# Kernel tuning notes

Hardware: AMD Instinct MI355X
Metric: run time of the kernel (lower is better)

## Reference

```python
import jax, jax.numpy as jnp
import numpy as np

D_MODEL = 1024
NUM_HEADS = 16
DEPTH = D_MODEL // NUM_HEADS
B, S = 2, 2048


def setup_inputs() -> dict:
    key = jax.random.key(0)
    ks = jax.random.split(key, 12)
    scale = 1.0 / np.sqrt(D_MODEL)
    inp = {
        'q': jax.random.normal(ks[0], (B, S, D_MODEL), dtype=jnp.float32),
        'k': jax.random.normal(ks[1], (B, S, D_MODEL), dtype=jnp.float32),
        'v': jax.random.normal(ks[2], (B, S, D_MODEL), dtype=jnp.float32),
        'mask': jnp.zeros((1, 1, S, S), dtype=jnp.float32),
        'wq': jax.random.normal(ks[3], (D_MODEL, D_MODEL), dtype=jnp.float32) * scale,
        'bq': jnp.zeros((D_MODEL,), dtype=jnp.float32),
        'wk': jax.random.normal(ks[4], (D_MODEL, D_MODEL), dtype=jnp.float32) * scale,
        'bk': jnp.zeros((D_MODEL,), dtype=jnp.float32),
        'wv': jax.random.normal(ks[5], (D_MODEL, D_MODEL), dtype=jnp.float32) * scale,
        'bv': jnp.zeros((D_MODEL,), dtype=jnp.float32),
        'wo': jax.random.normal(ks[6], (D_MODEL, D_MODEL), dtype=jnp.float32) * scale,
        'bo': jnp.zeros((D_MODEL,), dtype=jnp.float32),
    }
    return inp


def _split_heads(x):
    # [B, S, D] -> [B, H, S, depth]
    b, s, _ = x.shape
    return x.reshape(b, s, NUM_HEADS, DEPTH).transpose(0, 2, 1, 3)


def reference(q, k, v, mask, wq, bq, wk, bk, wv, bv, wo, bo):
    qh = _split_heads(q @ wq + bq)   # [B,H,S,depth]
    kh = _split_heads(k @ wk + bk)
    vh = _split_heads(v @ wv + bv)
    logits = jnp.einsum('bhqd,bhkd->bhqk', qh, kh) / jnp.sqrt(jnp.float32(DEPTH))
    logits = logits + mask * (-1e9)
    attn = jax.nn.softmax(logits, axis=-1)
    out = jnp.einsum('bhqk,bhkd->bhqd', attn, vh)  # [B,H,S,depth]
    out = out.transpose(0, 2, 1, 3).reshape(q.shape[0], -1, D_MODEL)
    return out @ wo + bo
```

## Files before the change

kernel.cpp:

```cpp
#include <hip/hip_runtime.h>

typedef unsigned short u16;
typedef unsigned int   u32;
typedef unsigned long long u64;
typedef short s16;

using f32x4  = __attribute__((ext_vector_type(4))) float;
using bf16x8 = __attribute__((ext_vector_type(8))) __bf16;
using bf16x4 = __attribute__((ext_vector_type(4))) __bf16;
using u16x8  = __attribute__((ext_vector_type(8))) u16;
using u16x4  = __attribute__((ext_vector_type(4))) u16;
using s16x4  = __attribute__((ext_vector_type(4))) s16;

#define LOG2E 1.4426950408889634f

__device__ __forceinline__ u16 f2bf(float f) {
  u32 u = __builtin_bit_cast(u32, f);
  u32 r = u + 0x7fffu + ((u >> 16) & 1u);
  return (u16)(r >> 16);
}

__device__ __forceinline__ float ex2(float x) {
#if __has_builtin(__builtin_amdgcn_exp2f)
  return __builtin_amdgcn_exp2f(x);
#else
  return exp2f(x);
#endif
}

__device__ __forceinline__ u16x4 pack4(float p0, float p1, float p2, float p3) {
  bf16x4 b = {(__bf16)p0, (__bf16)p1, (__bf16)p2, (__bf16)p3};
  return __builtin_bit_cast(u16x4, b);
}

__device__ __forceinline__ void gll16(const u16* g, u16* l) {
  __builtin_amdgcn_global_load_lds(
      (const __attribute__((address_space(1))) void*)g,
      (__attribute__((address_space(3))) void*)l, 16, 0, 0);
}

__device__ __forceinline__ bf16x8 ld_bf8(const u16* p) {
  return __builtin_bit_cast(bf16x8, *(const u16x8*)p);
}

__device__ __forceinline__ f32x4 mfma32(bf16x8 a, bf16x8 b, f32x4 c) {
  return __builtin_amdgcn_mfma_f32_16x16x32_bf16(a, b, c, 0, 0, 0);
}

#if __has_builtin(__builtin_amdgcn_mfma_f32_16x16x16bf16_1k)
__device__ __forceinline__ f32x4 pv_mfma(u16x4 a, u16x4 b, f32x4 c) {
  return __builtin_amdgcn_mfma_f32_16x16x16bf16_1k(
      __builtin_bit_cast(s16x4, a), __builtin_bit_cast(s16x4, b), c, 0, 0, 0);
}
#else
__device__ __forceinline__ f32x4 pv_mfma(u16x4 a, u16x4 b, f32x4 c) {
  u16x8 a8 = {a[0], a[1], a[2], a[3], 0, 0, 0, 0};
  u16x8 b8 = {b[0], b[1], b[2], b[3], 0, 0, 0, 0};
  return mfma32(__builtin_bit_cast(bf16x8, a8),
                __builtin_bit_cast(bf16x8, b8), c);
}
#endif

__global__ __launch_bounds__(256) void pre_kernel(
    const float* __restrict__ q, const float* __restrict__ k,
    const float* __restrict__ v, const float* __restrict__ mask,
    const float* __restrict__ wq, const float* __restrict__ wk,
    const float* __restrict__ wv, const float* __restrict__ wo,
    u16* __restrict__ qb, u16* __restrict__ kb, u16* __restrict__ vb,
    u16* __restrict__ wqT, u16* __restrict__ wkT, u16* __restrict__ wvT,
    u16* __restrict__ woT, int* flag) {
  int y = blockIdx.y, t = threadIdx.x;
  if (y < 3) {
    const float* src = y == 0 ? q : y == 1 ? k : v;
    u16* dst = y == 0 ? qb : y == 1 ? kb : vb;
    u64 i = ((u64)blockIdx.x * 256 + t) * 8;
    f32x4 a = *(const f32x4*)(src + i);
    f32x4 b = *(const f32x4*)(src + i + 4);
    u16x8 o;
    o[0] = f2bf(a[0]); o[1] = f2bf(a[1]); o[2] = f2bf(a[2]); o[3] = f2bf(a[3]);
    o[4] = f2bf(b[0]); o[5] = f2bf(b[1]); o[6] = f2bf(b[2]); o[7] = f2bf(b[3]);
    *(u16x8*)(dst + i) = o;
  } else if (y == 3) {
    __shared__ float tile[32][33];
    int x = t & 31, yy = t >> 5;
#pragma unroll
    for (int rep = 0; rep < 2; ++rep) {
      int job = blockIdx.x * 2 + rep;
      int z = job >> 10, tt = job & 1023;
      const float* W = z == 0 ? wq : z == 1 ? wk : z == 2 ? wv : wo;
      u16* WT = z == 0 ? wqT : z == 1 ? wkT : z == 2 ? wvT : woT;
      int c0 = (tt & 31) * 32, r0 = (tt >> 5) * 32;
#pragma unroll
      for (int j = 0; j < 4; ++j)
        tile[yy + j * 8][x] = W[(u64)(r0 + yy + j * 8) * 1024 + c0 + x];
      __syncthreads();
#pragma unroll
      for (int j = 0; j < 4; ++j)
        WT[(u64)(c0 + yy + j * 8) * 1024 + r0 + x] = f2bf(tile[x][yy + j * 8]);
      __syncthreads();
    }
  } else {
    u64 i = ((u64)blockIdx.x * 256 + t) * 8;
    f32x4 a = *(const f32x4*)(mask + i);
    f32x4 b = *(const f32x4*)(mask + i + 4);
    bool nz = a[0] != 0.f || a[1] != 0.f || a[2] != 0.f || a[3] != 0.f ||
              b[0] != 0.f || b[1] != 0.f || b[2] != 0.f || b[3] != 0.f;
    if (nz) atomicOr(flag, 1);
  }
}

__device__ __forceinline__ void gemm_core(const u16* __restrict__ A,
                                          const u16* __restrict__ Wt, int m0,
                                          int n0, u16* As, u16* Bs,
                                          f32x4 acc[4][4]) {
  int t = threadIdx.x, w = t >> 6, lane = t & 63;
  int quad = lane >> 4, l16 = lane & 15;
  int wr = w >> 1, wc = w & 1;
  for (int kt = 0; kt < 1024; kt += 64) {
#pragma unroll
    for (int j = 0; j < 4; ++j) {
      int g = j * 256 + t;
      int row = g >> 3, slot = g & 7;
      int cc = slot ^ (row & 7);
      gll16(A + (u64)(m0 + row) * 1024 + kt + cc * 8, &As[g * 8]);
      gll16(Wt + (u64)(n0 + row) * 1024 + kt + cc * 8, &Bs[g * 8]);
    }
    __syncthreads();
#pragma unroll
    for (int ks = 0; ks < 2; ++ks) {
      bf16x8 af[4], bfr[4];
#pragma unroll
      for (int mi = 0; mi < 4; ++mi) {
        int r = wr * 64 + mi * 16 + l16;
        af[mi] = ld_bf8(&As[(r * 8 + ((ks * 4 + quad) ^ (r & 7))) * 8]);
      }
#pragma unroll
      for (int ni = 0; ni < 4; ++ni) {
        int r = wc * 64 + ni * 16 + l16;
        bfr[ni] = ld_bf8(&Bs[(r * 8 + ((ks * 4 + quad) ^ (r & 7))) * 8]);
      }
#pragma unroll
      for (int mi = 0; mi < 4; ++mi)
#pragma unroll
        for (int ni = 0; ni < 4; ++ni)
          acc[mi][ni] = mfma32(af[mi], bfr[ni], acc[mi][ni]);
    }
    __syncthreads();
  }
}

__global__ __launch_bounds__(256) void qkv_gemm(
    const u16* __restrict__ qb, const u16* __restrict__ kb,
    const u16* __restrict__ vb, const u16* __restrict__ wqT,
    const u16* __restrict__ wkT, const u16* __restrict__ wvT,
    const float* __restrict__ bq, const float* __restrict__ bk,
    const float* __restrict__ bv, u16* __restrict__ Qh,
    u16* __restrict__ Khs, u16* __restrict__ Vhs) {
  int z = blockIdx.z;
  const u16* A = z == 0 ? qb : z == 1 ? kb : vb;
  const u16* Wt = z == 0 ? wqT : z == 1 ? wkT : wvT;
  const float* bias = z == 0 ? bq : z == 1 ? bk : bv;
  int m0 = blockIdx.x * 128, n0 = blockIdx.y * 128;
  __shared__ u16 SH[16384];
  f32x4 acc[4][4] = {};
  gemm_core(A, Wt, m0, n0, SH, SH + 8192, acc);
  int t = threadIdx.x, w = t >> 6, lane = t & 63;
  int quad = lane >> 4, l16 = lane & 15;
  int wr = w >> 1, wc = w & 1;
  int h = (n0 + wc * 64) >> 6;
  if (z == 2) {
#pragma unroll
    for (int mi = 0; mi < 4; ++mi) {
      int gm0 = m0 + wr * 64 + mi * 16;
      int bh = (gm0 >> 11) * 16 + h;
      int tIdx = (gm0 & 2047) >> 6;
      int kvq = ((gm0 & 63) >> 2) + quad;
      u16* tile = Vhs + ((u64)(bh * 32 + tIdx)) * 4096;
#pragma unroll
      for (int ni = 0; ni < 4; ++ni) {
        int d = ni * 16 + l16;
        float bv_ = bias[n0 + wc * 64 + d];
        u16x4 pv = pack4(acc[mi][ni][0] + bv_, acc[mi][ni][1] + bv_,
                         acc[mi][ni][2] + bv_, acc[mi][ni][3] + bv_);
        *(u16x4*)&tile[(kvq * 64 + d) * 4] = pv;
      }
    }
  } else {
    __syncthreads();
    u16* TB = SH + w * 2304;
    float scale = (z == 0) ? (LOG2E / 8.f) : 1.f;
#pragma unroll
    for (int p = 0; p < 2; ++p) {
#pragma unroll
      for (int mi2 = 0; mi2 < 2; ++mi2)
#pragma unroll
        for (int ni = 0; ni < 4; ++ni) {
          int d = ni * 16 + l16;
          float bv_ = bias[n0 + wc * 64 + d];
#pragma unroll
          for (int r = 0; r < 4; ++r) {
            int kvloc = mi2 * 16 + quad * 4 + r;
            TB[kvloc * 72 + d] =
                f2bf((acc[p * 2 + mi2][ni][r] + bv_) * scale);
          }
        }
      int gm0 = m0 + wr * 64 + p * 32;
      int bh = (gm0 >> 11) * 16 + h;
#pragma unroll
      for (int i = 0; i < 4; ++i) {
        int g = i * 64 + lane;
        int kvloc = g >> 3, slot = g & 7;
        if (z == 0) {
          u16x8 gran = *(u16x8*)&TB[kvloc * 72 + slot * 8];
          int s = (gm0 & 2047) + kvloc;
          *(u16x8*)&Qh[((u64)bh * 2048 + s) * 64 + slot * 8] = gran;
        } else {
          u16x8 gran = *(u16x8*)&TB[kvloc * 72 + (slot ^ (kvloc & 7)) * 8];
          int tIdx = (gm0 & 2047) >> 6;
          int kv = (gm0 & 63) + kvloc;
          *(u16x8*)&Khs[((u64)(bh * 32 + tIdx)) * 4096 + kv * 64 + slot * 8] =
              gran;
        }
      }
    }
  }
}

template <int CUR>
__device__ __forceinline__ void fa_fast_step(
    int T, int t, int quad, int l16, int hf, int x7,
    const u16* __restrict__ Kg0, const u16* __restrict__ Vg0, u16* Kb0,
    u16* Vb0, bf16x8 aq0, bf16x8 aq1, f32x4 (&o)[4], f32x4& l_acc,
    const u16x4 ones) {
  if (T + 1 < 32) {
    gll16(Kg0 + (u64)(T + 1) * 4096 + t * 8, &Kb0[(CUR ^ 1) * 4096 + t * 8]);
    gll16(Vg0 + (u64)(T + 1) * 4096 + t * 8, &Vb0[(CUR ^ 1) * 4096 + t * 8]);
  }
  const u16* Kt = Kb0 + CUR * 4096;
  const u16* Vt = Vb0 + CUR * 4096;
  u16x4 pk[2];
#pragma unroll
  for (int c = 0; c < 2; ++c) {
    int kvr = hf * 32 + c * 16 + l16;
    bf16x8 k0 = ld_bf8(&Kt[kvr * 64 + ((quad ^ x7)) * 8]);
    bf16x8 k1 = ld_bf8(&Kt[kvr * 64 + (((quad + 4) ^ x7)) * 8]);
    f32x4 s_ = {};
    s_ = mfma32(k0, aq0, s_);
    s_ = mfma32(k1, aq1, s_);
    pk[c] = pack4(ex2(s_[0]), ex2(s_[1]), ex2(s_[2]), ex2(s_[3]));
  }
#pragma unroll
  for (int c = 0; c < 2; ++c) {
    int cc = hf * 2 + c;
    l_acc = pv_mfma(pk[c], ones, l_acc);
#pragma unroll
    for (int nt = 0; nt < 4; ++nt) {
      u16x4 vf =
          *(const u16x4*)&Vt[(((cc * 4 + quad) * 64) + nt * 16 + l16) * 4];
      o[nt] = pv_mfma(pk[c], vf, o[nt]);
    }
  }
  __syncthreads();
}

template <int CUR>
__device__ __forceinline__ void fa_mask_step(
    int T, int t, int lane, int quad, int l16, int hf, int x7, int qg,
    const u16* __restrict__ Kg0, const u16* __restrict__ Vg0,
    const float* __restrict__ mask, u16* Kb0, u16* Vb0, bf16x8 aq0,
    bf16x8 aq1, f32x4 (&o)[4], float& m_r, float& l_r) {
  if (T + 1 < 32) {
    gll16(Kg0 + (u64)(T + 1) * 4096 + t * 8, &Kb0[(CUR ^ 1) * 4096 + t * 8]);
    gll16(Vg0 + (u64)(T + 1) * 4096 + t * 8, &Vb0[(CUR ^ 1) * 4096 + t * 8]);
  }
  const u16* Kt = Kb0 + CUR * 4096;
  const u16* Vt = Vb0 + CUR * 4096;
  f32x4 sv[2];
#pragma unroll
  for (int c = 0; c < 2; ++c) {
    int kvr = hf * 32 + c * 16 + l16;
    bf16x8 k0 = ld_bf8(&Kt[kvr * 64 + ((quad ^ x7)) * 8]);
    bf16x8 k1 = ld_bf8(&Kt[kvr * 64 + (((quad + 4) ^ x7)) * 8]);
    f32x4 s_ = {};
    s_ = mfma32(k0, aq0, s_);
    s_ = mfma32(k1, aq1, s_);
    sv[c] = s_;
  }
#pragma unroll
  for (int c = 0; c < 2; ++c)
#pragma unroll
    for (int r = 0; r < 4; ++r)
      sv[c][r] += mask[(u64)qg * 2048 + T * 64 + hf * 32 + c * 16 + quad * 4 +
                       r] *
                  (-1e9f * LOG2E);
  float mx = fmaxf(fmaxf(fmaxf(sv[0][0], sv[0][1]), fmaxf(sv[0][2], sv[0][3])),
                   fmaxf(fmaxf(sv[1][0], sv[1][1]), fmaxf(sv[1][2], sv[1][3])));
  mx = fmaxf(mx, __shfl_xor(mx, 16));
  mx = fmaxf(mx, __shfl_xor(mx, 32));
  float mnew = fmaxf(m_r, mx);
  float alpha = ex2(m_r - mnew);
  m_r = mnew;
  float rs = 0.f;
  u16x4 pk[2];
#pragma unroll
  for (int c = 0; c < 2; ++c) {
    float p0 = ex2(sv[c][0] - m_r), p1 = ex2(sv[c][1] - m_r);
    float p2 = ex2(sv[c][2] - m_r), p3 = ex2(sv[c][3] - m_r);
    rs += (p0 + p1) + (p2 + p3);
    pk[c] = pack4(p0, p1, p2, p3);
  }
  rs += __shfl_xor(rs, 16);
  rs += __shfl_xor(rs, 32);
  l_r = l_r * alpha + rs;
  float a4[4];
#pragma unroll
  for (int r = 0; r < 4; ++r)
    a4[r] = __shfl(alpha, (lane & 48) | (quad * 4 + r));
#pragma unroll
  for (int nt = 0; nt < 4; ++nt)
#pragma unroll
    for (int r = 0; r < 4; ++r) o[nt][r] *= a4[r];
#pragma unroll
  for (int c = 0; c < 2; ++c) {
    int cc = hf * 2 + c;
#pragma unroll
    for (int nt = 0; nt < 4; ++nt) {
      u16x4 vf =
          *(const u16x4*)&Vt[(((cc * 4 + quad) * 64) + nt * 16 + l16) * 4];
      o[nt] = pv_mfma(pk[c], vf, o[nt]);
    }
  }
  __syncthreads();
}

__global__ __launch_bounds__(512, 8) void flash_attn(
    const u16* __restrict__ Qh, const u16* __restrict__ Khs,
    const u16* __restrict__ Vhs, const float* __restrict__ mask,
    const int* __restrict__ flag, u16* __restrict__ Ob) {
  int L = blockIdx.x + (blockIdx.y << 5);
  int bh = (L & 7) * 4 + ((L >> 3) & 3);
  int q0 = (L >> 5) * 64;
  int t = threadIdx.x, w = t >> 6, lane = t & 63;
  int quad = lane >> 4, l16 = lane & 15;
  int s = w >> 1, hf = w & 1;
  __shared__ u16 SMEM[16384];
  u16* Kb0 = SMEM;
  u16* Vb0 = SMEM + 8192;
  const u16* Kg0 = Khs + (u64)bh * 32 * 4096;
  const u16* Vg0 = Vhs + (u64)bh * 32 * 4096;
  const u16* Qbase = Qh + ((u64)bh * 2048 + q0 + s * 16 + l16) * 64 + quad * 8;
  bf16x8 aq0 = ld_bf8(Qbase);
  bf16x8 aq1 = ld_bf8(Qbase + 32);
  f32x4 o[4] = {};
  const bool use_mask = (*flag) != 0;
  int x7 = l16 & 7;
  const u16x4 ones = {0x3F80, 0x3F80, 0x3F80, 0x3F80};
  gll16(Kg0 + t * 8, &Kb0[t * 8]);
  gll16(Vg0 + t * 8, &Vb0[t * 8]);
  __syncthreads();
  int b = bh >> 4, h = bh & 15;
  float* scratch = (float*)SMEM;
  float* my = scratch + (s * 64 + lane) * 20;
  if (!use_mask) {
    f32x4 l_acc = {};
    for (int T = 0; T < 32; T += 2) {
      fa_fast_step<0>(T, t, quad, l16, hf, x7, Kg0, Vg0, Kb0, Vb0, aq0, aq1,
                      o, l_acc, ones);
      fa_fast_step<1>(T + 1, t, quad, l16, hf, x7, Kg0, Vg0, Kb0, Vb0, aq0,
                      aq1, o, l_acc, ones);
    }
    if (hf) {
#pragma unroll
      for (int nt = 0; nt < 4; ++nt)
#pragma unroll
        for (int r = 0; r < 4; ++r) my[nt * 4 + r] = o[nt][r];
#pragma unroll
      for (int r = 0; r < 4; ++r) my[16 + r] = l_acc[r];
    }
    __syncthreads();
    if (!hf) {
      float rl[4];
#pragma unroll
      for (int r = 0; r < 4; ++r) rl[r] = 1.f / (l_acc[r] + my[16 + r]);
#pragma unroll
      for (int nt = 0; nt < 4; ++nt)
#pragma unroll
        for (int r = 0; r < 4; ++r) {
          int srow = q0 + s * 16 + quad * 4 + r;
          Ob[(u64)(b * 2048 + srow) * 1024 + h * 64 + nt * 16 + l16] =
              f2bf((o[nt][r] + my[nt * 4 + r]) * rl[r]);
        }
    }
  } else {
    float m_r = -1e30f, l_r = 0.f;
    int qg = q0 + s * 16 + l16;
    for (int T = 0; T < 32; T += 2) {
      fa_mask_step<0>(T, t, lane, quad, l16, hf, x7, qg, Kg0, Vg0, mask, Kb0,
                      Vb0, aq0, aq1, o, m_r, l_r);
      fa_mask_step<1>(T + 1, t, lane, quad, l16, hf, x7, qg, Kg0, Vg0, mask,
                      Kb0, Vb0, aq0, aq1, o, m_r, l_r);
    }
    if (hf) {
#pragma unroll
      for (int nt = 0; nt < 4; ++nt)
#pragma unroll
        for (int r = 0; r < 4; ++r) my[nt * 4 + r] = o[nt][r];
      my[16] = l_r;
      my[17] = m_r;
    }
    __syncthreads();
    if (!hf) {
      float l1 = my[16], m1 = my[17];
      float m = fmaxf(m_r, m1);
      float c0 = ex2(m_r - m), c1 = ex2(m1 - m);
      float l = l_r * c0 + l1 * c1;
      float c0r[4], c1r[4], rl[4];
#pragma unroll
      for (int r = 0; r < 4; ++r) {
        int src = (lane & 48) | (quad * 4 + r);
        c0r[r] = __shfl(c0, src);
        c1r[r] = __shfl(c1, src);
        rl[r] = 1.f / __shfl(l, src);
      }
#pragma unroll
      for (int nt = 0; nt < 4; ++nt)
#pragma unroll
        for (int r = 0; r < 4; ++r) {
          int srow = q0 + s * 16 + quad * 4 + r;
          float val = (o[nt][r] * c0r[r] + my[nt * 4 + r] * c1r[r]) * rl[r];
          Ob[(u64)(b * 2048 + srow) * 1024 + h * 64 + nt * 16 + l16] =
              f2bf(val);
        }
    }
  }
}

__global__ __launch_bounds__(256) void out_gemm(const u16* __restrict__ Ob,
                                                const u16* __restrict__ woT,
                                                const float* __restrict__ bo,
                                                float* __restrict__ out) {
  int m0 = blockIdx.x * 128, n0 = blockIdx.y * 64;
  __shared__ u16 As[128 * 64], Bs[64 * 64];
  f32x4 acc[2][4] = {};
  int t = threadIdx.x, w = t >> 6, lane = t & 63;
  int quad = lane >> 4, l16 = lane & 15;
  for (int kt = 0; kt < 1024; kt += 64) {
#pragma unroll
    for (int j = 0; j < 4; ++j) {
      int g = j * 256 + t;
      int row = g >> 3, slot = g & 7;
      int cc = slot ^ (row & 7);
      gll16(Ob + (u64)(m0 + row) * 1024 + kt + cc * 8, &As[g * 8]);
    }
#pragma unroll
    for (int j = 0; j < 2; ++j) {
      int g = j * 256 + t;
      int row = g >> 3, slot = g & 7;
      int cc = slot ^ (row & 7);
      gll16(woT + (u64)(n0 + row) * 1024 + kt + cc * 8, &Bs[g * 8]);
    }
    __syncthreads();
#pragma unroll
    for (int ks = 0; ks < 2; ++ks) {
      bf16x8 af[2], bfr[4];
#pragma unroll
      for (int mi = 0; mi < 2; ++mi) {
        int r = w * 32 + mi * 16 + l16;
        af[mi] = ld_bf8(&As[(r * 8 + ((ks * 4 + quad) ^ (r & 7))) * 8]);
      }
#pragma unroll
      for (int ni = 0; ni < 4; ++ni) {
        int r = ni * 16 + l16;
        bfr[ni] = ld_bf8(&Bs[(r * 8 + ((ks * 4 + quad) ^ (r & 7))) * 8]);
      }
#pragma unroll
      for (int mi = 0; mi < 2; ++mi)
#pragma unroll
        for (int ni = 0; ni < 4; ++ni)
          acc[mi][ni] = mfma32(af[mi], bfr[ni], acc[mi][ni]);
    }
    __syncthreads();
  }
#pragma unroll
  for (int mi = 0; mi < 2; ++mi) {
#pragma unroll
    for (int ni = 0; ni < 4; ++ni) {
      int gn = n0 + ni * 16 + l16;
      float bv_ = bo[gn];
#pragma unroll
      for (int r = 0; r < 4; ++r) {
        int gm = m0 + w * 32 + mi * 16 + quad * 4 + r;
        out[(u64)gm * 1024 + gn] = acc[mi][ni][r] + bv_;
      }
    }
  }
}

extern "C" void kernel_launch(void* const* d_in, const int* in_sizes, int n_in,
                              void* d_out, int out_size, void* d_ws,
                              size_t ws_size, hipStream_t stream) {
  const float* q = (const float*)d_in[0];
  const float* k = (const float*)d_in[1];
  const float* v = (const float*)d_in[2];
  const float* mask = (const float*)d_in[3];
  const float* wq = (const float*)d_in[4];
  const float* bq = (const float*)d_in[5];
  const float* wk = (const float*)d_in[6];
  const float* bk = (const float*)d_in[7];
  const float* wv = (const float*)d_in[8];
  const float* bv = (const float*)d_in[9];
  const float* wo = (const float*)d_in[10];
  const float* bo = (const float*)d_in[11];
  float* out = (float*)d_out;
  char* ws = (char*)d_ws;
  const u64 MB = 1ull << 20;
  u16* qb = (u16*)(ws + 0 * MB);
  u16* kb = (u16*)(ws + 8 * MB);
  u16* vb = (u16*)(ws + 16 * MB);
  u16* wqT = (u16*)(ws + 24 * MB);
  u16* wkT = (u16*)(ws + 26 * MB);
  u16* wvT = (u16*)(ws + 28 * MB);
  u16* woT = (u16*)(ws + 30 * MB);
  u16* Qh = (u16*)(ws + 32 * MB);
  u16* Khs = (u16*)(ws + 40 * MB);
  u16* Vhs = (u16*)(ws + 48 * MB);
  int* flag = (int*)(ws + 56 * MB);
  u16* Ob = qb;

  hipMemsetAsync(flag, 0, 4, stream);
  pre_kernel<<<dim3(2048, 5), 256, 0, stream>>>(
      q, k, v, mask, wq, wk, wv, wo, qb, kb, vb, wqT, wkT, wvT, woT, flag);
  qkv_gemm<<<dim3(32, 8, 3), 256, 0, stream>>>(qb, kb, vb, wqT, wkT, wvT, bq,
                                               bk, bv, Qh, Khs, Vhs);
  flash_attn<<<dim3(32, 32), 512, 0, stream>>>(Qh, Khs, Vhs, mask, flag, Ob);
  out_gemm<<<dim3(32, 16), 256, 0, stream>>>(Ob, woT, bo, out);
}
```

Baseline: 237.1 us.

## Make each flash-attention wave cover full KV tile and double queries per block

Each wave in flash_attn now processes all 64 keys of a KV tile for its own 16 query rows, instead of two waves splitting each tile in half. A block therefore covers 128 queries, and the grid is halved. This halves K/V tile loads per query and removes the shared-memory merge of partial outputs and softmax statistics at the end. It also raises wave priority around the PV MFMA section and relaxes the occupancy hint in launch_bounds. The trade-off is fewer blocks in flight and more work and register pressure per wave.

Result: faster. 232.0 us (-2.1%).

```diff
diff --git a/kernel.cpp b/kernel.cpp
--- a/kernel.cpp
+++ b/kernel.cpp
@@ -228,7 +228,7 @@
 
 template <int CUR>
 __device__ __forceinline__ void fa_fast_step(
-    int T, int t, int quad, int l16, int hf, int x7,
+    int T, int t, int quad, int l16, int x7,
     const u16* __restrict__ Kg0, const u16* __restrict__ Vg0, u16* Kb0,
     u16* Vb0, bf16x8 aq0, bf16x8 aq1, f32x4 (&o)[4], f32x4& l_acc,
     const u16x4 ones) {
@@ -238,34 +238,35 @@
   }
   const u16* Kt = Kb0 + CUR * 4096;
   const u16* Vt = Vb0 + CUR * 4096;
-  u16x4 pk[2];
-#pragma unroll
-  for (int c = 0; c < 2; ++c) {
-    int kvr = hf * 32 + c * 16 + l16;
+  u16x4 pk[4];
+#pragma unroll
+  for (int cc = 0; cc < 4; ++cc) {
+    int kvr = cc * 16 + l16;
     bf16x8 k0 = ld_bf8(&Kt[kvr * 64 + ((quad ^ x7)) * 8]);
     bf16x8 k1 = ld_bf8(&Kt[kvr * 64 + (((quad + 4) ^ x7)) * 8]);
     f32x4 s_ = {};
     s_ = mfma32(k0, aq0, s_);
     s_ = mfma32(k1, aq1, s_);
-    pk[c] = pack4(ex2(s_[0]), ex2(s_[1]), ex2(s_[2]), ex2(s_[3]));
-  }
-#pragma unroll
-  for (int c = 0; c < 2; ++c) {
-    int cc = hf * 2 + c;
-    l_acc = pv_mfma(pk[c], ones, l_acc);
+    pk[cc] = pack4(ex2(s_[0]), ex2(s_[1]), ex2(s_[2]), ex2(s_[3]));
+  }
+  __builtin_amdgcn_s_setprio(1);
+#pragma unroll
+  for (int cc = 0; cc < 4; ++cc) {
+    l_acc = pv_mfma(pk[cc], ones, l_acc);
 #pragma unroll
     for (int nt = 0; nt < 4; ++nt) {
       u16x4 vf =
           *(const u16x4*)&Vt[(((cc * 4 + quad) * 64) + nt * 16 + l16) * 4];
-      o[nt] = pv_mfma(pk[c], vf, o[nt]);
-    }
-  }
+      o[nt] = pv_mfma(pk[cc], vf, o[nt]);
+    }
+  }
+  __builtin_amdgcn_s_setprio(0);
   __syncthreads();
 }
 
 template <int CUR>
 __device__ __forceinline__ void fa_mask_step(
-    int T, int t, int lane, int quad, int l16, int hf, int x7, int qg,
+    int T, int t, int lane, int quad, int l16, int x7, int qg,
     const u16* __restrict__ Kg0, const u16* __restrict__ Vg0,
     const float* __restrict__ mask, u16* Kb0, u16* Vb0, bf16x8 aq0,
     bf16x8 aq1, f32x4 (&o)[4], float& m_r, float& l_r) {
@@ -275,39 +276,41 @@
   }
   const u16* Kt = Kb0 + CUR * 4096;
   const u16* Vt = Vb0 + CUR * 4096;
-  f32x4 sv[2];
-#pragma unroll
-  for (int c = 0; c < 2; ++c) {
-    int kvr = hf * 32 + c * 16 + l16;
+  f32x4 sv[4];
+#pragma unroll
+  for (int cc = 0; cc < 4; ++cc) {
+    int kvr = cc * 16 + l16;
     bf16x8 k0 = ld_bf8(&Kt[kvr * 64 + ((quad ^ x7)) * 8]);
     bf16x8 k1 = ld_bf8(&Kt[kvr * 64 + (((quad + 4) ^ x7)) * 8]);
     f32x4 s_ = {};
     s_ = mfma32(k0, aq0, s_);
     s_ = mfma32(k1, aq1, s_);
-    sv[c] = s_;
-  }
-#pragma unroll
-  for (int c = 0; c < 2; ++c)
+    sv[cc] = s_;
+  }
+#pragma unroll
+  for (int cc = 0; cc < 4; ++cc)
 #pragma unroll
     for (int r = 0; r < 4; ++r)
-      sv[c][r] += mask[(u64)qg * 2048 + T * 64 + hf * 32 + c * 16 + quad * 4 +
-                       r] *
-                  (-1e9f * LOG2E);
-  float mx = fmaxf(fmaxf(fmaxf(sv[0][0], sv[0][1]), fmaxf(sv[0][2], sv[0][3])),
-                   fmaxf(fmaxf(sv[1][0], sv[1][1]), fmaxf(sv[1][2], sv[1][3])));
+      sv[cc][r] += mask[(u64)qg * 2048 + T * 64 + cc * 16 + quad * 4 + r] *
+                   (-1e9f * LOG2E);
+  float mx = -1e30f;
+#pragma unroll
+  for (int cc = 0; cc < 4; ++cc)
+    mx = fmaxf(mx, fmaxf(fmaxf(sv[cc][0], sv[cc][1]),
+                         fmaxf(sv[cc][2], sv[cc][3])));
   mx = fmaxf(mx, __shfl_xor(mx, 16));
   mx = fmaxf(mx, __shfl_xor(mx, 32));
   float mnew = fmaxf(m_r, mx);
   float alpha = ex2(m_r - mnew);
   m_r = mnew;
   float rs = 0.f;
-  u16x4 pk[2];
-#pragma unroll
-  for (int c = 0; c < 2; ++c) {
-    float p0 = ex2(sv[c][0] - m_r), p1 = ex2(sv[c][1] - m_r);
-    float p2 = ex2(sv[c][2] - m_r), p3 = ex2(sv[c][3] - m_r);
+  u16x4 pk[4];
+#pragma unroll
+  for (int cc = 0; cc < 4; ++cc) {
+    float p0 = ex2(sv[cc][0] - m_r), p1 = ex2(sv[cc][1] - m_r);
+    float p2 = ex2(sv[cc][2] - m_r), p3 = ex2(sv[cc][3] - m_r);
     rs += (p0 + p1) + (p2 + p3);
-    pk[c] = pack4(p0, p1, p2, p3);
+    pk[cc] = pack4(p0, p1, p2, p3);
   }
   rs += __shfl_xor(rs, 16);
   rs += __shfl_xor(rs, 32);
@@ -320,35 +323,35 @@
   for (int nt = 0; nt < 4; ++nt)
 #pragma unroll
     for (int r = 0; r < 4; ++r) o[nt][r] *= a4[r];
-#pragma unroll
-  for (int c = 0; c < 2; ++c) {
-    int cc = hf * 2 + c;
+  __builtin_amdgcn_s_setprio(1);
+#pragma unroll
+  for (int cc = 0; cc < 4; ++cc) {
 #pragma unroll
     for (int nt = 0; nt < 4; ++nt) {
       u16x4 vf =
           *(const u16x4*)&Vt[(((cc * 4 + quad) * 64) + nt * 16 + l16) * 4];
-      o[nt] = pv_mfma(pk[c], vf, o[nt]);
-    }
-  }
+      o[nt] = pv_mfma(pk[cc], vf, o[nt]);
+    }
+  }
+  __builtin_amdgcn_s_setprio(0);
   __syncthreads();
 }
 
-__global__ __launch_bounds__(512, 8) void flash_attn(
+__global__ __launch_bounds__(512, 4) void flash_attn(
     const u16* __restrict__ Qh, const u16* __restrict__ Khs,
     const u16* __restrict__ Vhs, const float* __restrict__ mask,
     const int* __restrict__ flag, u16* __restrict__ Ob) {
-  int L = blockIdx.x + (blockIdx.y << 5);
+  int L = blockIdx.x + (blockIdx.y << 4);
   int bh = (L & 7) * 4 + ((L >> 3) & 3);
-  int q0 = (L >> 5) * 64;
+  int q0 = (L >> 5) * 128;
   int t = threadIdx.x, w = t >> 6, lane = t & 63;
   int quad = lane >> 4, l16 = lane & 15;
-  int s = w >> 1, hf = w & 1;
   __shared__ u16 SMEM[16384];
   u16* Kb0 = SMEM;
   u16* Vb0 = SMEM + 8192;
   const u16* Kg0 = Khs + (u64)bh * 32 * 4096;
   const u16* Vg0 = Vhs + (u64)bh * 32 * 4096;
-  const u16* Qbase = Qh + ((u64)bh * 2048 + q0 + s * 16 + l16) * 64 + quad * 8;
+  const u16* Qbase = Qh + ((u64)bh * 2048 + q0 + w * 16 + l16) * 64 + quad * 8;
   bf16x8 aq0 = ld_bf8(Qbase);
   bf16x8 aq1 = ld_bf8(Qbase + 32);
   f32x4 o[4] = {};
@@ -359,79 +362,46 @@
   gll16(Vg0 + t * 8, &Vb0[t * 8]);
   __syncthreads();
   int b = bh >> 4, h = bh & 15;
-  float* scratch = (float*)SMEM;
-  float* my = scratch + (s * 64 + lane) * 20;
   if (!use_mask) {
     f32x4 l_acc = {};
     for (int T = 0; T < 32; T += 2) {
-      fa_fast_step<0>(T, t, quad, l16, hf, x7, Kg0, Vg0, Kb0, Vb0, aq0, aq1,
+      fa_fast_step<0>(T, t, quad, l16, x7, Kg0, Vg0, Kb0, Vb0, aq0, aq1, o,
+                      l_acc, ones);
+      fa_fast_step<1>(T + 1, t, quad, l16, x7, Kg0, Vg0, Kb0, Vb0, aq0, aq1,
                       o, l_acc, ones);
-      fa_fast_step<1>(T + 1, t, quad, l16, hf, x7, Kg0, Vg0, Kb0, Vb0, aq0,
-                      aq1, o, l_acc, ones);
-    }
-    if (hf) {
-#pragma unroll
-      for (int nt = 0; nt < 4; ++nt)
-#pragma unroll
-        for (int r = 0; r < 4; ++r) my[nt * 4 + r] = o[nt][r];
-#pragma unroll
-      for (int r = 0; r < 4; ++r) my[16 + r] = l_acc[r];
-    }
-    __syncthreads();
-    if (!hf) {
-      float rl[4];
-#pragma unroll
-      for (int r = 0; r < 4; ++r) rl[r] = 1.f / (l_acc[r] + my[16 + r]);
-#pragma unroll
-      for (int nt = 0; nt < 4; ++nt)
-#pragma unroll
-        for (int r = 0; r < 4; ++r) {
-          int srow = q0 + s * 16 + quad * 4 + r;
-          Ob[(u64)(b * 2048 + srow) * 1024 + h * 64 + nt * 16 + l16] =
-              f2bf((o[nt][r] + my[nt * 4 + r]) * rl[r]);
-        }
-    }
+    }
+    float rl[4];
+#pragma unroll
+    for (int r = 0; r < 4; ++r) rl[r] = 1.f / l_acc[r];
+#pragma unroll
+    for (int nt = 0; nt < 4; ++nt)
+#pragma unroll
+      for (int r = 0; r < 4; ++r) {
+        int srow = q0 + w * 16 + quad * 4 + r;
+        Ob[(u64)(b * 2048 + srow) * 1024 + h * 64 + nt * 16 + l16] =
+            f2bf(o[nt][r] * rl[r]);
+      }
   } else {
     float m_r = -1e30f, l_r = 0.f;
-    int qg = q0 + s * 16 + l16;
+    int qg = q0 + w * 16 + l16;
     for (int T = 0; T < 32; T += 2) {
-      fa_mask_step<0>(T, t, lane, quad, l16, hf, x7, qg, Kg0, Vg0, mask, Kb0,
+      fa_mask_step<0>(T, t, lane, quad, l16, x7, qg, Kg0, Vg0, mask, Kb0, Vb0,
+                      aq0, aq1, o, m_r, l_r);
+      fa_mask_step<1>(T + 1, t, lane, quad, l16, x7, qg, Kg0, Vg0, mask, Kb0,
                       Vb0, aq0, aq1, o, m_r, l_r);
-      fa_mask_step<1>(T + 1, t, lane, quad, l16, hf, x7, qg, Kg0, Vg0, mask,
-                      Kb0, Vb0, aq0, aq1, o, m_r, l_r);
-    }
-    if (hf) {
-#pragma unroll
-      for (int nt = 0; nt < 4; ++nt)
-#pragma unroll
-        for (int r = 0; r < 4; ++r) my[nt * 4 + r] = o[nt][r];
-      my[16] = l_r;
-      my[17] = m_r;
-    }
-    __syncthreads();
-    if (!hf) {
-      float l1 = my[16], m1 = my[17];
-      float m = fmaxf(m_r, m1);
-      float c0 = ex2(m_r - m), c1 = ex2(m1 - m);
-      float l = l_r * c0 + l1 * c1;
-      float c0r[4], c1r[4], rl[4];
+    }
+    float rl[4];
+#pragma unroll
+    for (int r = 0; r < 4; ++r)
+      rl[r] = 1.f / __shfl(l_r, (lane & 48) | (quad * 4 + r));
+#pragma unroll
+    for (int nt = 0; nt < 4; ++nt)
 #pragma unroll
       for (int r = 0; r < 4; ++r) {
-        int src = (lane & 48) | (quad * 4 + r);
-        c0r[r] = __shfl(c0, src);
-        c1r[r] = __shfl(c1, src);
-        rl[r] = 1.f / __shfl(l, src);
-      }
-#pragma unroll
-      for (int nt = 0; nt < 4; ++nt)
-#pragma unroll
-        for (int r = 0; r < 4; ++r) {
-          int srow = q0 + s * 16 + quad * 4 + r;
-          float val = (o[nt][r] * c0r[r] + my[nt * 4 + r] * c1r[r]) * rl[r];
-          Ob[(u64)(b * 2048 + srow) * 1024 + h * 64 + nt * 16 + l16] =
-              f2bf(val);
-        }
-    }
+        int srow = q0 + w * 16 + quad * 4 + r;
+        Ob[(u64)(b * 2048 + srow) * 1024 + h * 64 + nt * 16 + l16] =
+            f2bf(o[nt][r] * rl[r]);
+      }
   }
 }
 
@@ -532,6 +502,6 @@
       q, k, v, mask, wq, wk, wv, wo, qb, kb, vb, wqT, wkT, wvT, woT, flag);
   qkv_gemm<<<dim3(32, 8, 3), 256, 0, stream>>>(qb, kb, vb, wqT, wkT, wvT, bq,
                                                bk, bv, Qh, Khs, Vhs);
-  flash_attn<<<dim3(32, 32), 512, 0, stream>>>(Qh, Khs, Vhs, mask, flag, Ob);
+  flash_attn<<<dim3(16, 32), 512, 0, stream>>>(Qh, Khs, Vhs, mask, flag, Ob);
   out_gemm<<<dim3(32, 16), 256, 0, stream>>>(Ob, woT, bo, out);
 }
```
